# Kernel tuning notes

Hardware: AMD Instinct MI355X
Metric: run time of the kernel (lower is better)

## Reference

```python
import jax, jax.numpy as jnp
import numpy as np

EPS = 1e-4


def setup_inputs() -> dict:
    key = jax.random.key(0)
    ks = jax.random.split(key, 16)
    N, D, H, K = 262144, 162, 256, 30
    s = 0.05  # weight init scale
    return {
        "Yh": jax.random.uniform(ks[0], (N, D), dtype=jnp.float32),
        "u": jax.random.uniform(ks[1], (1,), dtype=jnp.float32),
        "W1": jax.random.normal(ks[2], (D, H), dtype=jnp.float32) * s,
        "b1": jnp.zeros((H,), jnp.float32),
        "W2": jax.random.normal(ks[3], (H, H), dtype=jnp.float32) * s,
        "b2": jnp.zeros((H,), jnp.float32),
        "Wa": jax.random.normal(ks[4], (H, K), dtype=jnp.float32) * s,
        "ba": jnp.zeros((K,), jnp.float32),
        "Wb": jax.random.normal(ks[5], (H, K), dtype=jnp.float32) * s,
        "bb": jnp.zeros((K,), jnp.float32),
        "Wd1": jax.random.normal(ks[6], (K, H), dtype=jnp.float32) * s,
        "bd1": jnp.zeros((H,), jnp.float32),
        "Wd2": jax.random.normal(ks[7], (H, D), dtype=jnp.float32) * s,
        "bd2": jnp.zeros((D,), jnp.float32),
    }


def _stick_segments(v):
    # pi_k = v_k * prod_{j<k} (1 - v_j)  (vectorized exclusive cumprod,
    # replacing the original per-dim Python loop)
    cp = jnp.cumprod(1.0 - v, axis=1)  # [N, K]
    excl = jnp.concatenate([jnp.ones_like(v[:, :1]), cp[:, :-1]], axis=1)
    return v * excl


def reference(Yh, u, W1, b1, W2, b2, Wa, ba, Wb, bb, Wd1, bd1, Wd2, bd2):
    # encode_hsi: dense MLP -> positive Kumaraswamy params (softplus heads)
    h = jax.nn.relu(Yh @ W1 + b1)
    h = jax.nn.relu(h @ W2 + b2)
    alpha = jax.nn.softplus(h @ Wa + ba) + EPS  # param1_hsi [N, K]
    beta = jax.nn.softplus(h @ Wb + bb) + EPS   # param2_hsi [N, K]
    # Kumaraswamy reparametrization with a single shared uniform sample
    uu = u[0] * 0.98 + 0.01  # Uniform(0.01, 0.99) scalar
    v = (1.0 - uu ** (1.0 / beta)) ** (1.0 / alpha)  # [N, K]
    # set_v_K_to_one: force last stick proportion to 1
    v = jnp.concatenate([v[:, :-1], jnp.ones_like(v[:, :1])], axis=1)
    pi_h = _stick_segments(v)  # [N, K], rows sum to 1
    # decode: MLP -> sigmoid (positive outputs, recon.log() finite)
    d = jax.nn.relu(pi_h @ Wd1 + bd1)
    recon = jax.nn.sigmoid(d @ Wd2 + bd2)  # [N, D]
    return recon, alpha, beta, pi_h
```

## Files before the change

kernel.cpp:

```cpp
#include <hip/hip_runtime.h>
#include <hip/hip_bf16.h>

#define N_ROWS 262144
#define D_IN 162
#define K_DIM 30
#define ROWS 64
#define NTHR 256

using bf16_t = __hip_bfloat16;
typedef __attribute__((ext_vector_type(8))) short bf16x8;
typedef __attribute__((ext_vector_type(4))) float f32x4;

__device__ __forceinline__ int swz_byte(int row, int col) {
  int b = (row << 9) + (col << 1);
  return b ^ ((row & 7) << 4);
}

__device__ __forceinline__ uint32_t bf16b(float x) {
  return (uint32_t)__builtin_bit_cast(unsigned short, __float2bfloat16(x));
}
__device__ __forceinline__ uint32_t pack2(float lo, float hi) {
  return bf16b(lo) | (bf16b(hi) << 16);
}
__device__ __forceinline__ float unpk_lo(uint32_t p) {
  return __bfloat162float(__builtin_bit_cast(__hip_bfloat16, (unsigned short)(p & 0xffff)));
}
__device__ __forceinline__ float unpk_hi(uint32_t p) {
  return __bfloat162float(__builtin_bit_cast(__hip_bfloat16, (unsigned short)(p >> 16)));
}

__device__ __forceinline__ float fexp2(float x) { return __builtin_amdgcn_exp2f(x); }
__device__ __forceinline__ float flog2(float x) { return __builtin_amdgcn_logf(x); }
__device__ __forceinline__ float frcp (float x) { return __builtin_amdgcn_rcpf(x); }

__device__ __forceinline__ float sp_fast(float x) {
  float e = fexp2(fabsf(x) * -1.44269504f);
  return fmaxf(x, 0.f) + 0.69314718f * flog2(1.f + e);
}
__device__ __forceinline__ float sigmoid_fast(float x) {
  return frcp(1.f + fexp2(x * -1.44269504f));
}

__global__ void pack_b_kernel(const float* __restrict__ src, bf16_t* __restrict__ dst,
                              int K, int N, int Np, int KB) {
  int idx = blockIdx.x * 256 + threadIdx.x;
  int total = KB * Np * 32;
  if (idx >= total) return;
  int ks = idx & 31;
  int n  = (idx >> 5) % Np;
  int kb = idx / (32 * Np);
  int k  = kb * 32 + ks;
  float v = (k < K && n < N) ? src[k * N + n] : 0.f;
  dst[idx] = __float2bfloat16(v);
}

__global__ void pack_ab_kernel(const float* __restrict__ Wa, const float* __restrict__ Wb,
                               bf16_t* __restrict__ dst) {
  int idx = blockIdx.x * 256 + threadIdx.x;
  if (idx >= 8 * 64 * 32) return;
  int ks = idx & 31;
  int n  = (idx >> 5) & 63;
  int kb = idx >> 11;
  int k  = kb * 32 + ks;
  int j = n >> 1, s = n & 1;
  float v = (j < K_DIM) ? (s ? Wb[k * K_DIM + j] : Wa[k * K_DIM + j]) : 0.f;
  dst[idx] = __float2bfloat16(v);
}

template<int NP, int NMO>
__device__ __forceinline__ void wload(const bf16_t* __restrict__ Wp, int kb, int ocBase,
                                      int lr, int lg, bf16x8 (&out)[NMO]) {
#pragma unroll
  for (int mo = 0; mo < NMO; ++mo)
    out[mo] = *reinterpret_cast<const bf16x8*>(
        Wp + ((kb * NP + ocBase + 16 * mo + lr) << 5) + 8 * lg);
}

template<int KB, int NP, int NMO, int NR>
__device__ __forceinline__ void gemm_direct(const uint8_t* lds, int srcOff,
                                            const bf16_t* __restrict__ Wp, int ocBase,
                                            int lr, int lg, f32x4 (&acc)[NMO][NR]) {
  int bE[NR], bO[NR];
#pragma unroll
  for (int nr = 0; nr < NR; ++nr) {
    bE[nr] = srcOff + swz_byte(16 * nr + lr, 8 * lg);
    bO[nr] = srcOff + swz_byte(16 * nr + lr, 32 + 8 * lg);
  }
#pragma unroll
  for (int kb = 0; kb < KB; ++kb) {
    bf16x8 wf[NMO];
    wload<NP, NMO>(Wp, kb, ocBase, lr, lg, wf);
    bf16x8 hf[NR];
#pragma unroll
    for (int nr = 0; nr < NR; ++nr) {
      int base = (kb & 1) ? bO[nr] : bE[nr];
      hf[nr] = *reinterpret_cast<const bf16x8*>(lds + base + (kb >> 1) * 128);
    }
#pragma unroll
    for (int mo = 0; mo < NMO; ++mo)
#pragma unroll
      for (int nr = 0; nr < NR; ++nr)
        acc[mo][nr] = __builtin_amdgcn_mfma_f32_16x16x32_bf16(wf[mo], hf[nr], acc[mo][nr], 0, 0, 0);
  }
}

template<int NMO, int NR>
__device__ __forceinline__ void acc_bias_init(const float* __restrict__ bias, int ocBase,
                                              int lg, f32x4 (&acc)[NMO][NR]) {
#pragma unroll
  for (int mo = 0; mo < NMO; ++mo) {
    float4 bv = *reinterpret_cast<const float4*>(bias + ocBase + 16 * mo + 4 * lg);
    f32x4 t = {bv.x, bv.y, bv.z, bv.w};
#pragma unroll
    for (int nr = 0; nr < NR; ++nr) acc[mo][nr] = t;
  }
}

template<int NMO, int NR>
__device__ __forceinline__ void epi_relu_store(uint8_t* lds, int dstOff, int ocBase,
                                               int lr, int lg, f32x4 (&acc)[NMO][NR]) {
#pragma unroll
  for (int mo = 0; mo < NMO; ++mo)
#pragma unroll
    for (int nr = 0; nr < NR; ++nr) {
      int row = 16 * nr + lr;
      int col = ocBase + 16 * mo + 4 * lg;
      float x0 = fmaxf(acc[mo][nr][0], 0.f), x1 = fmaxf(acc[mo][nr][1], 0.f);
      float x2 = fmaxf(acc[mo][nr][2], 0.f), x3 = fmaxf(acc[mo][nr][3], 0.f);
      uint2 p; p.x = pack2(x0, x1); p.y = pack2(x2, x3);
      *reinterpret_cast<uint2*>(lds + dstOff + swz_byte(row, col)) = p;
    }
}

template<int LG>
__device__ __forceinline__ bf16x8 scan_frag(const float* __restrict__ vrow,
                                            uint8_t* __restrict__ piPair) {
  float ex = 1.f, hold = 0.f;
  uint32_t pk0 = 0, pk1 = 0, pk2 = 0, pk3 = 0;
#pragma unroll
  for (int j = 0; j < 32; ++j) {
    float pi;
    if (j < K_DIM - 1)       { float vj = vrow[j]; pi = vj * ex; ex *= (1.f - vj); }
    else if (j == K_DIM - 1)   pi = ex;
    else                       pi = 0.f;
    if (j & 1) {
      uint32_t p = pack2(hold, pi);
      if (piPair != nullptr && j < K_DIM)
        *reinterpret_cast<uint32_t*>(piPair + (j - 1) * 2) = p;
      if (j >= 8 * LG && j < 8 * LG + 8) {
        switch ((j - 8 * LG) >> 1) {
          case 0: pk0 = p; break; case 1: pk1 = p; break;
          case 2: pk2 = p; break; default: pk3 = p;
        }
      }
    } else hold = pi;
  }
  uint4 t = make_uint4(pk0, pk1, pk2, pk3);
  return __builtin_bit_cast(bf16x8, t);
}

#define OFF_PI 32768

__launch_bounds__(NTHR, 4)
__global__ void usdn_fused(const float* __restrict__ Yh, const float* __restrict__ u,
                           const float* __restrict__ b1, const float* __restrict__ b2,
                           const float* __restrict__ ba, const float* __restrict__ bb,
                           const float* __restrict__ bd1, const float* __restrict__ bd2,
                           const bf16_t* __restrict__ Wp1, const bf16_t* __restrict__ Wp2,
                           const bf16_t* __restrict__ Wpab, const bf16_t* __restrict__ Wpd1,
                           const bf16_t* __restrict__ Wpd2,
                           float* __restrict__ outRecon, float* __restrict__ outAlpha,
                           float* __restrict__ outBeta, float* __restrict__ outPi) {
  __shared__ __align__(16) uint8_t lds[37888];

  const int tid = threadIdx.x;
  const int w  = tid >> 6;
  const int l  = tid & 63;
  const int lr = l & 15;
  const int lg = l >> 4;
  const int r0 = blockIdx.x * ROWS;

  {
    const int srow = tid >> 2, sl4 = tid & 3;
    const float2* src = reinterpret_cast<const float2*>(Yh + (size_t)(r0 + srow) * D_IN);
#pragma unroll
    for (int h = 0; h < 3; ++h) {
      float2 sv[8];
#pragma unroll
      for (int it = 0; it < 8; ++it) {
        int f2 = sl4 + (h * 8 + it) * 4;
        if (f2 < 81) sv[it] = src[f2];
      }
#pragma unroll
      for (int it = 0; it < 8; ++it) {
        int f2 = sl4 + (h * 8 + it) * 4;
        uint32_t p = 0;
        if (f2 < 81) p = pack2(sv[it].x, sv[it].y);
        *reinterpret_cast<uint32_t*>(lds + swz_byte(srow, f2 * 2)) = p;
      }
    }
  }
  __syncthreads();

  {
    f32x4 acc[4][4];
    acc_bias_init<4, 4>(b1, w * 64, lg, acc);
    gemm_direct<6, 256, 4, 4>(lds, 0, Wp1, w * 64, lr, lg, acc);
    __syncthreads();
    epi_relu_store<4, 4>(lds, 0, w * 64, lr, lg, acc);
  }
  __syncthreads();

  {
    f32x4 acc[4][4];
    acc_bias_init<4, 4>(b2, w * 64, lg, acc);
    gemm_direct<8, 256, 4, 4>(lds, 0, Wp2, w * 64, lr, lg, acc);
    __syncthreads();
    epi_relu_store<4, 4>(lds, 0, w * 64, lr, lg, acc);
  }
  __syncthreads();

  float regA[4][2], regB[4][2];
  const int j0 = 8 * w + 2 * lg;
  {
    bool jv = (j0 < K_DIM);
    float ba0 = jv ? ba[j0] : 0.f,     bb0 = jv ? bb[j0] : 0.f;
    float ba1 = jv ? ba[j0 + 1] : 0.f, bb1 = jv ? bb[j0 + 1] : 0.f;
    f32x4 acc[1][4];
    f32x4 binit = {ba0, bb0, ba1, bb1};
#pragma unroll
    for (int nr = 0; nr < 4; ++nr) acc[0][nr] = binit;
    gemm_direct<8, 64, 1, 4>(lds, 0, Wpab, 16 * w, lr, lg, acc);

    float uu  = u[0] * 0.98f + 0.01f;
    float l2u = flog2(uu);
    float vv[4][2];
#pragma unroll
    for (int nr = 0; nr < 4; ++nr) {
      float a0  = sp_fast(acc[0][nr][0]) + 1e-4f;
      float b0v = sp_fast(acc[0][nr][1]) + 1e-4f;
      float a1  = sp_fast(acc[0][nr][2]) + 1e-4f;
      float b1v = sp_fast(acc[0][nr][3]) + 1e-4f;
      regA[nr][0] = a0; regB[nr][0] = b0v;
      regA[nr][1] = a1; regB[nr][1] = b1v;
      float t0 = fexp2(l2u * frcp(b0v));
      vv[nr][0] = fexp2(flog2(1.f - t0) * frcp(a0));
      float t1 = fexp2(l2u * frcp(b1v));
      vv[nr][1] = fexp2(flog2(1.f - t1) * frcp(a1));
    }
    __syncthreads();
    float* vbuf = reinterpret_cast<float*>(lds);
    if (jv) {
#pragma unroll
      for (int nr = 0; nr < 4; ++nr) {
        int row = 16 * nr + lr;
        if (j0 < K_DIM - 1)     vbuf[row * 33 + j0]     = vv[nr][0];
        if (j0 + 1 < K_DIM - 1) vbuf[row * 33 + j0 + 1] = vv[nr][1];
      }
    }
  }
  __syncthreads();

  {
    bf16x8 pf[4];
    const float* vb = reinterpret_cast<const float*>(lds);
#pragma unroll
    for (int nr = 0; nr < 4; ++nr) {
      int row = 16 * nr + lr;
      const float* vrow = vb + row * 33;
      uint8_t* po = (w == 0) ? (lds + OFF_PI + row * 80) : nullptr;
      if      (lg == 0) pf[nr] = scan_frag<0>(vrow, po);
      else if (lg == 1) pf[nr] = scan_frag<1>(vrow, nullptr);
      else if (lg == 2) pf[nr] = scan_frag<2>(vrow, nullptr);
      else              pf[nr] = scan_frag<3>(vrow, nullptr);
    }
    f32x4 acc[4][4];
    acc_bias_init<4, 4>(bd1, w * 64, lg, acc);
    bf16x8 w4[4];
    wload<256, 4>(Wpd1, 0, w * 64, lr, lg, w4);
#pragma unroll
    for (int mo = 0; mo < 4; ++mo)
#pragma unroll
      for (int nr = 0; nr < 4; ++nr)
        acc[mo][nr] = __builtin_amdgcn_mfma_f32_16x16x32_bf16(w4[mo], pf[nr], acc[mo][nr], 0, 0, 0);
    __syncthreads();
    epi_relu_store<4, 4>(lds, 0, w * 64, lr, lg, acc);
  }
  __syncthreads();

  {
    f32x4 acc[3][4];
#pragma unroll
    for (int mo = 0; mo < 3; ++mo) {
      int col0 = 48 * w + 16 * mo + 4 * lg;
      f32x4 t;
#pragma unroll
      for (int i = 0; i < 4; ++i) t[i] = (col0 + i < D_IN) ? bd2[col0 + i] : 0.f;
#pragma unroll
      for (int nr = 0; nr < 4; ++nr) acc[mo][nr] = t;
    }
    gemm_direct<8, 192, 3, 4>(lds, 0, Wpd2, 48 * w, lr, lg, acc);
#pragma unroll
    for (int mo = 0; mo < 3; ++mo) {
      int col0 = 48 * w + 16 * mo + 4 * lg;
#pragma unroll
      for (int nr = 0; nr < 4; ++nr) {
        int row = 16 * nr + lr;
        float s0 = sigmoid_fast(acc[mo][nr][0]);
        float s1 = sigmoid_fast(acc[mo][nr][1]);
        float s2 = sigmoid_fast(acc[mo][nr][2]);
        float s3 = sigmoid_fast(acc[mo][nr][3]);
        float* dst = outRecon + (size_t)(r0 + row) * D_IN + col0;
        if (col0 < D_IN)     *reinterpret_cast<float2*>(dst)     = make_float2(s0, s1);
        if (col0 + 2 < D_IN) *reinterpret_cast<float2*>(dst + 2) = make_float2(s2, s3);
      }
    }
  }

  if (j0 < K_DIM) {
#pragma unroll
    for (int nr = 0; nr < 4; ++nr) {
      int row = 16 * nr + lr;
      size_t base = (size_t)(r0 + row) * K_DIM + j0;
      *reinterpret_cast<float2*>(outAlpha + base) = make_float2(regA[nr][0], regA[nr][1]);
      *reinterpret_cast<float2*>(outBeta  + base) = make_float2(regB[nr][0], regB[nr][1]);
    }
  }
  {
    int row = tid >> 2, l4 = tid & 3;
#pragma unroll
    for (int it = 0; it < 4; ++it) {
      int f2 = l4 + it * 4;
      if (f2 < 15) {
        uint32_t pp = *reinterpret_cast<const uint32_t*>(lds + OFF_PI + row * 80 + f2 * 4);
        *reinterpret_cast<float2*>(outPi + (size_t)(r0 + row) * K_DIM + f2 * 2) =
            make_float2(unpk_lo(pp), unpk_hi(pp));
      }
    }
  }
}

extern "C" void kernel_launch(void* const* d_in, const int* in_sizes, int n_in,
                              void* d_out, int out_size, void* d_ws, size_t ws_size,
                              hipStream_t stream) {
  const float* Yh  = (const float*)d_in[0];
  const float* u   = (const float*)d_in[1];
  const float* W1  = (const float*)d_in[2];
  const float* b1  = (const float*)d_in[3];
  const float* W2  = (const float*)d_in[4];
  const float* b2  = (const float*)d_in[5];
  const float* Wa  = (const float*)d_in[6];
  const float* ba  = (const float*)d_in[7];
  const float* Wb  = (const float*)d_in[8];
  const float* bb  = (const float*)d_in[9];
  const float* Wd1 = (const float*)d_in[10];
  const float* bd1 = (const float*)d_in[11];
  const float* Wd2 = (const float*)d_in[12];
  const float* bd2 = (const float*)d_in[13];

  bf16_t* ws   = (bf16_t*)d_ws;
  bf16_t* Wp1  = ws;
  bf16_t* Wp2  = Wp1 + 49152;
  bf16_t* Wpab = Wp2 + 65536;
  bf16_t* Wpd1 = Wpab + 16384;
  bf16_t* Wpd2 = Wpd1 + 8192;

  float* outRecon = (float*)d_out;
  float* outAlpha = outRecon + (size_t)N_ROWS * D_IN;
  float* outBeta  = outAlpha + (size_t)N_ROWS * K_DIM;
  float* outPi    = outBeta  + (size_t)N_ROWS * K_DIM;

  pack_b_kernel<<<192, 256, 0, stream>>>(W1, Wp1, 162, 256, 256, 6);
  pack_b_kernel<<<256, 256, 0, stream>>>(W2, Wp2, 256, 256, 256, 8);
  pack_ab_kernel<<<64, 256, 0, stream>>>(Wa, Wb, Wpab);
  pack_b_kernel<<<32, 256, 0, stream>>>(Wd1, Wpd1, 30, 256, 256, 1);
  pack_b_kernel<<<192, 256, 0, stream>>>(Wd2, Wpd2, 256, 162, 192, 8);

  usdn_fused<<<N_ROWS / ROWS, NTHR, 0, stream>>>(Yh, u, b1, b2, ba, bb, bd1, bd2,
                                                 Wp1, Wp2, Wpab, Wpd1, Wpd2,
                                                 outRecon, outAlpha, outBeta, outPi);
}
```

Baseline: 299.5 us.

## Halve rows per block, double waves, and ping-pong LDS to drop syncs

Each block now handles 32 rows with 512 threads (8 waves), so every wave computes a 32-column slice with 2x2 MFMA tiles instead of 4x4, and launch bounds now ask for 8 blocks per CU. The first two MLP layers alternate between two LDS regions (offset 0 and OFF_B), which removes the barrier that used to sit between each GEMM and its epilogue store. Some stages now run on only part of the waves (heads on 4, decoder output on 6). This cuts registers per thread and raises occupancy, at the cost of more blocks, less reuse of each weight fragment across rows, and idle waves in those later stages.

Result: faster. 278.8 us (-6.9%).

```diff
diff --git a/kernel.cpp b/kernel.cpp
--- a/kernel.cpp
+++ b/kernel.cpp
@@ -4,8 +4,8 @@
 #define N_ROWS 262144
 #define D_IN 162
 #define K_DIM 30
-#define ROWS 64
-#define NTHR 256
+#define ROWS 32
+#define NTHR 512
 
 using bf16_t = __hip_bfloat16;
 typedef __attribute__((ext_vector_type(8))) short bf16x8;
@@ -159,9 +159,10 @@
   return __builtin_bit_cast(bf16x8, t);
 }
 
+#define OFF_B  16384
 #define OFF_PI 32768
 
-__launch_bounds__(NTHR, 4)
+__launch_bounds__(NTHR, 8)
 __global__ void usdn_fused(const float* __restrict__ Yh, const float* __restrict__ u,
                            const float* __restrict__ b1, const float* __restrict__ b2,
                            const float* __restrict__ ba, const float* __restrict__ bb,
@@ -171,7 +172,7 @@
                            const bf16_t* __restrict__ Wpd2,
                            float* __restrict__ outRecon, float* __restrict__ outAlpha,
                            float* __restrict__ outBeta, float* __restrict__ outPi) {
-  __shared__ __align__(16) uint8_t lds[37888];
+  __shared__ __align__(16) uint8_t lds[35328];
 
   const int tid = threadIdx.x;
   const int w  = tid >> 6;
@@ -181,19 +182,19 @@
   const int r0 = blockIdx.x * ROWS;
 
   {
-    const int srow = tid >> 2, sl4 = tid & 3;
+    const int srow = tid >> 4, s16 = tid & 15;
     const float2* src = reinterpret_cast<const float2*>(Yh + (size_t)(r0 + srow) * D_IN);
 #pragma unroll
-    for (int h = 0; h < 3; ++h) {
-      float2 sv[8];
-#pragma unroll
-      for (int it = 0; it < 8; ++it) {
-        int f2 = sl4 + (h * 8 + it) * 4;
+    for (int h = 0; h < 2; ++h) {
+      float2 sv[3];
+#pragma unroll
+      for (int it = 0; it < 3; ++it) {
+        int f2 = s16 + (h * 3 + it) * 16;
         if (f2 < 81) sv[it] = src[f2];
       }
 #pragma unroll
-      for (int it = 0; it < 8; ++it) {
-        int f2 = sl4 + (h * 8 + it) * 4;
+      for (int it = 0; it < 3; ++it) {
+        int f2 = s16 + (h * 3 + it) * 16;
         uint32_t p = 0;
         if (f2 < 81) p = pack2(sv[it].x, sv[it].y);
         *reinterpret_cast<uint32_t*>(lds + swz_byte(srow, f2 * 2)) = p;
@@ -203,69 +204,63 @@
   __syncthreads();
 
   {
-    f32x4 acc[4][4];
-    acc_bias_init<4, 4>(b1, w * 64, lg, acc);
-    gemm_direct<6, 256, 4, 4>(lds, 0, Wp1, w * 64, lr, lg, acc);
-    __syncthreads();
-    epi_relu_store<4, 4>(lds, 0, w * 64, lr, lg, acc);
+    f32x4 acc[2][2];
+    acc_bias_init<2, 2>(b1, w * 32, lg, acc);
+    gemm_direct<6, 256, 2, 2>(lds, 0, Wp1, w * 32, lr, lg, acc);
+    epi_relu_store<2, 2>(lds, OFF_B, w * 32, lr, lg, acc);
   }
   __syncthreads();
 
   {
-    f32x4 acc[4][4];
-    acc_bias_init<4, 4>(b2, w * 64, lg, acc);
-    gemm_direct<8, 256, 4, 4>(lds, 0, Wp2, w * 64, lr, lg, acc);
-    __syncthreads();
-    epi_relu_store<4, 4>(lds, 0, w * 64, lr, lg, acc);
-  }
-  __syncthreads();
-
-  float regA[4][2], regB[4][2];
+    f32x4 acc[2][2];
+    acc_bias_init<2, 2>(b2, w * 32, lg, acc);
+    gemm_direct<8, 256, 2, 2>(lds, OFF_B, Wp2, w * 32, lr, lg, acc);
+    epi_relu_store<2, 2>(lds, 0, w * 32, lr, lg, acc);
+  }
+  __syncthreads();
+
+  float regA[2][2], regB[2][2];
   const int j0 = 8 * w + 2 * lg;
-  {
+  if (w < 4) {
     bool jv = (j0 < K_DIM);
     float ba0 = jv ? ba[j0] : 0.f,     bb0 = jv ? bb[j0] : 0.f;
     float ba1 = jv ? ba[j0 + 1] : 0.f, bb1 = jv ? bb[j0 + 1] : 0.f;
-    f32x4 acc[1][4];
+    f32x4 acc[1][2];
     f32x4 binit = {ba0, bb0, ba1, bb1};
-#pragma unroll
-    for (int nr = 0; nr < 4; ++nr) acc[0][nr] = binit;
-    gemm_direct<8, 64, 1, 4>(lds, 0, Wpab, 16 * w, lr, lg, acc);
+    acc[0][0] = binit; acc[0][1] = binit;
+    gemm_direct<8, 64, 1, 2>(lds, 0, Wpab, 16 * w, lr, lg, acc);
 
     float uu  = u[0] * 0.98f + 0.01f;
     float l2u = flog2(uu);
-    float vv[4][2];
-#pragma unroll
-    for (int nr = 0; nr < 4; ++nr) {
+    float* vbuf = reinterpret_cast<float*>(lds + OFF_B);
+#pragma unroll
+    for (int nr = 0; nr < 2; ++nr) {
+      int row = 16 * nr + lr;
       float a0  = sp_fast(acc[0][nr][0]) + 1e-4f;
       float b0v = sp_fast(acc[0][nr][1]) + 1e-4f;
       float a1  = sp_fast(acc[0][nr][2]) + 1e-4f;
       float b1v = sp_fast(acc[0][nr][3]) + 1e-4f;
       regA[nr][0] = a0; regB[nr][0] = b0v;
       regA[nr][1] = a1; regB[nr][1] = b1v;
-      float t0 = fexp2(l2u * frcp(b0v));
-      vv[nr][0] = fexp2(flog2(1.f - t0) * frcp(a0));
-      float t1 = fexp2(l2u * frcp(b1v));
-      vv[nr][1] = fexp2(flog2(1.f - t1) * frcp(a1));
-    }
-    __syncthreads();
-    float* vbuf = reinterpret_cast<float*>(lds);
-    if (jv) {
-#pragma unroll
-      for (int nr = 0; nr < 4; ++nr) {
-        int row = 16 * nr + lr;
-        if (j0 < K_DIM - 1)     vbuf[row * 33 + j0]     = vv[nr][0];
-        if (j0 + 1 < K_DIM - 1) vbuf[row * 33 + j0 + 1] = vv[nr][1];
+      if (jv) {
+        if (j0 < K_DIM - 1) {
+          float t = fexp2(l2u * frcp(b0v));
+          vbuf[row * 33 + j0] = fexp2(flog2(1.f - t) * frcp(a0));
+        }
+        if (j0 + 1 < K_DIM - 1) {
+          float t = fexp2(l2u * frcp(b1v));
+          vbuf[row * 33 + j0 + 1] = fexp2(flog2(1.f - t) * frcp(a1));
+        }
       }
     }
   }
   __syncthreads();
 
   {
-    bf16x8 pf[4];
-    const float* vb = reinterpret_cast<const float*>(lds);
-#pragma unroll
-    for (int nr = 0; nr < 4; ++nr) {
+    bf16x8 pf[2];
+    const float* vb = reinterpret_cast<const float*>(lds + OFF_B);
+#pragma unroll
+    for (int nr = 0; nr < 2; ++nr) {
       int row = 16 * nr + lr;
       const float* vrow = vb + row * 33;
       uint8_t* po = (w == 0) ? (lds + OFF_PI + row * 80) : nullptr;
@@ -274,37 +269,36 @@
       else if (lg == 2) pf[nr] = scan_frag<2>(vrow, nullptr);
       else              pf[nr] = scan_frag<3>(vrow, nullptr);
     }
-    f32x4 acc[4][4];
-    acc_bias_init<4, 4>(bd1, w * 64, lg, acc);
-    bf16x8 w4[4];
-    wload<256, 4>(Wpd1, 0, w * 64, lr, lg, w4);
-#pragma unroll
-    for (int mo = 0; mo < 4; ++mo)
-#pragma unroll
-      for (int nr = 0; nr < 4; ++nr)
+    f32x4 acc[2][2];
+    acc_bias_init<2, 2>(bd1, w * 32, lg, acc);
+    bf16x8 w4[2];
+    wload<256, 2>(Wpd1, 0, w * 32, lr, lg, w4);
+#pragma unroll
+    for (int mo = 0; mo < 2; ++mo)
+#pragma unroll
+      for (int nr = 0; nr < 2; ++nr)
         acc[mo][nr] = __builtin_amdgcn_mfma_f32_16x16x32_bf16(w4[mo], pf[nr], acc[mo][nr], 0, 0, 0);
-    __syncthreads();
-    epi_relu_store<4, 4>(lds, 0, w * 64, lr, lg, acc);
-  }
-  __syncthreads();
-
-  {
-    f32x4 acc[3][4];
-#pragma unroll
-    for (int mo = 0; mo < 3; ++mo) {
-      int col0 = 48 * w + 16 * mo + 4 * lg;
+    epi_relu_store<2, 2>(lds, 0, w * 32, lr, lg, acc);
+  }
+  __syncthreads();
+
+  if (w < 6) {
+    f32x4 acc[2][2];
+#pragma unroll
+    for (int mo = 0; mo < 2; ++mo) {
+      int col0 = 32 * w + 16 * mo + 4 * lg;
       f32x4 t;
 #pragma unroll
       for (int i = 0; i < 4; ++i) t[i] = (col0 + i < D_IN) ? bd2[col0 + i] : 0.f;
 #pragma unroll
-      for (int nr = 0; nr < 4; ++nr) acc[mo][nr] = t;
-    }
-    gemm_direct<8, 192, 3, 4>(lds, 0, Wpd2, 48 * w, lr, lg, acc);
-#pragma unroll
-    for (int mo = 0; mo < 3; ++mo) {
-      int col0 = 48 * w + 16 * mo + 4 * lg;
-#pragma unroll
-      for (int nr = 0; nr < 4; ++nr) {
+      for (int nr = 0; nr < 2; ++nr) acc[mo][nr] = t;
+    }
+    gemm_direct<8, 192, 2, 2>(lds, 0, Wpd2, 32 * w, lr, lg, acc);
+#pragma unroll
+    for (int mo = 0; mo < 2; ++mo) {
+      int col0 = 32 * w + 16 * mo + 4 * lg;
+#pragma unroll
+      for (int nr = 0; nr < 2; ++nr) {
         int row = 16 * nr + lr;
         float s0 = sigmoid_fast(acc[mo][nr][0]);
         float s1 = sigmoid_fast(acc[mo][nr][1]);
@@ -317,16 +311,16 @@
     }
   }
 
-  if (j0 < K_DIM) {
-#pragma unroll
-    for (int nr = 0; nr < 4; ++nr) {
+  if (w < 4 && j0 < K_DIM) {
+#pragma unroll
+    for (int nr = 0; nr < 2; ++nr) {
       int row = 16 * nr + lr;
       size_t base = (size_t)(r0 + row) * K_DIM + j0;
       *reinterpret_cast<float2*>(outAlpha + base) = make_float2(regA[nr][0], regA[nr][1]);
       *reinterpret_cast<float2*>(outBeta  + base) = make_float2(regB[nr][0], regB[nr][1]);
     }
   }
-  {
+  if (tid < 128) {
     int row = tid >> 2, l4 = tid & 3;
 #pragma unroll
     for (int it = 0; it < 4; ++it) {
```
